# Performance work log

Hardware: AMD Instinct MI355X
Metric: run time of the kernel (lower is better)

The kernel has to match this reference:

```python
import jax, jax.numpy as jnp
import numpy as np

NUM_BINS = 16

def _compute_histogram(colors, num_bins=NUM_BINS):
    # colors: (N, 3) in [0, 1]
    quantized = (colors * (num_bins - 1)).astype(jnp.int32)
    quantized = jnp.clip(quantized, 0, num_bins - 1)
    # flatten 3D bin index: r*B^2 + g*B + b
    flat_idx = (quantized[:, 0] * num_bins + quantized[:, 1]) * num_bins + quantized[:, 2]
    hist = jax.ops.segment_sum(
        jnp.ones(colors.shape[0], dtype=colors.dtype),
        flat_idx,
        num_segments=num_bins ** 3,
    )
    hist = hist / (hist.sum() + 1e-8)
    return hist  # (num_bins^3,)

def setup_inputs() -> dict:
    key = jax.random.key(0)
    k1, k2 = jax.random.split(key)
    source_colors = jax.random.uniform(k1, (8388608, 3), dtype=jnp.float32)
    target_palette = jax.random.uniform(k2, (4096, 3), dtype=jnp.float32)
    return {"source_colors": source_colors, "target_palette": target_palette}

def reference(source_colors, target_palette):
    source_hist = _compute_histogram(source_colors)
    target_hist = _compute_histogram(target_palette)
    loss = jnp.abs(source_hist - target_hist).mean()
    return loss
```

## Files before the change

kernel.cpp:

```cpp
#include <hip/hip_runtime.h>

#define BINS 4096

__device__ __forceinline__ int qz(float c) {
    int q = (int)(c * 15.0f);
    q = q < 0 ? 0 : q;
    q = q > 15 ? 15 : q;
    return q;
}

__device__ __forceinline__ int bin3(float r, float g, float b) {
    return (qz(r) * 16 + qz(g)) * 16 + qz(b);
}

__global__ __launch_bounds__(256) void src_hist_kernel(const float* __restrict__ src,
                                                       unsigned int* __restrict__ g_hist,
                                                       int n_pts) {
    __shared__ unsigned int lhist[BINS];
    for (int i = threadIdx.x; i < BINS; i += blockDim.x) lhist[i] = 0;
    __syncthreads();

    const float4* __restrict__ src4 = (const float4*)src;
    const int n_quads = n_pts >> 2;
    const int tid = blockIdx.x * blockDim.x + threadIdx.x;
    const int stride = gridDim.x * blockDim.x;

    for (int q = tid; q < n_quads; q += stride) {
        float4 a = src4[3 * q + 0];
        float4 b = src4[3 * q + 1];
        float4 c = src4[3 * q + 2];
        atomicAdd(&lhist[bin3(a.x, a.y, a.z)], 1u);
        atomicAdd(&lhist[bin3(a.w, b.x, b.y)], 1u);
        atomicAdd(&lhist[bin3(b.z, b.w, c.x)], 1u);
        atomicAdd(&lhist[bin3(c.y, c.z, c.w)], 1u);
    }

    if (blockIdx.x == 0) {
        int tail = n_pts & 3;
        if ((int)threadIdx.x < tail) {
            int p = (n_quads << 2) + threadIdx.x;
            atomicAdd(&lhist[bin3(src[3 * p], src[3 * p + 1], src[3 * p + 2])], 1u);
        }
    }

    __syncthreads();
    for (int i = threadIdx.x; i < BINS; i += blockDim.x) {
        unsigned int v = lhist[i];
        if (v) atomicAdd(&g_hist[i], v);
    }
}

__global__ __launch_bounds__(512) void loss_kernel(const float* __restrict__ tgt,
                                                   const unsigned int* __restrict__ g_hist,
                                                   float* __restrict__ out,
                                                   int n_src, int n_tgt) {
    __shared__ unsigned int thist[BINS];
    for (int i = threadIdx.x; i < BINS; i += blockDim.x) thist[i] = 0;
    __syncthreads();

    const float4* __restrict__ t4 = (const float4*)tgt;
    const int n_quads = n_tgt >> 2;
    for (int q = threadIdx.x; q < n_quads; q += blockDim.x) {
        float4 a = t4[3 * q + 0];
        float4 b = t4[3 * q + 1];
        float4 c = t4[3 * q + 2];
        atomicAdd(&thist[bin3(a.x, a.y, a.z)], 1u);
        atomicAdd(&thist[bin3(a.w, b.x, b.y)], 1u);
        atomicAdd(&thist[bin3(b.z, b.w, c.x)], 1u);
        atomicAdd(&thist[bin3(c.y, c.z, c.w)], 1u);
    }
    {
        int tail = n_tgt & 3;
        if ((int)threadIdx.x < tail) {
            int p = (n_quads << 2) + threadIdx.x;
            atomicAdd(&thist[bin3(tgt[3 * p], tgt[3 * p + 1], tgt[3 * p + 2])], 1u);
        }
    }
    __syncthreads();

    const double ns = (double)n_src + 1e-8;
    const double nt = (double)n_tgt + 1e-8;
    double acc = 0.0;
    for (int i = threadIdx.x; i < BINS; i += blockDim.x) {
        double s = (double)g_hist[i] / ns;
        double t = (double)thist[i] / nt;
        acc += fabs(s - t);
    }

    for (int off = 32; off > 0; off >>= 1) acc += __shfl_down(acc, off);
    __shared__ double red[8];
    const int lane = threadIdx.x & 63;
    const int wave = threadIdx.x >> 6;
    if (lane == 0) red[wave] = acc;
    __syncthreads();
    if (threadIdx.x == 0) {
        double s = 0.0;
        const int nwaves = (int)(blockDim.x >> 6);
        for (int w = 0; w < nwaves; ++w) s += red[w];
        out[0] = (float)(s / (double)BINS);
    }
}

extern "C" void kernel_launch(void* const* d_in, const int* in_sizes, int n_in,
                              void* d_out, int out_size, void* d_ws, size_t ws_size,
                              hipStream_t stream) {
    const float* src = (const float*)d_in[0];
    const float* tgt = (const float*)d_in[1];
    const int n_src = in_sizes[0] / 3;
    const int n_tgt = in_sizes[1] / 3;

    unsigned int* g_hist = (unsigned int*)d_ws;

    hipMemsetAsync(g_hist, 0, BINS * sizeof(unsigned int), stream);
    src_hist_kernel<<<1024, 256, 0, stream>>>(src, g_hist, n_src);
    loss_kernel<<<1, 512, 0, stream>>>(tgt, g_hist, (float*)d_out, n_src, n_tgt);
}
```

Baseline: 164.5 us.

## Fuse source histogram and loss into one kernel with last-block finalize

Merges the two kernels into a single launch. The last block to finish, found through an atomic counter and threadfence, builds the target histogram and computes the loss. The grid changes from 1024x256 to 256x512, and each block's flush into the global histogram starts at a rotated offset to spread atomic contention across bins. This removes one kernel launch and the gap between kernels. In exchange it adds a serialized tail on a single block plus the fence and counter overhead.

Result: slower. 176.1 us (+7.0%).

```diff
diff --git a/kernel.cpp b/kernel.cpp
--- a/kernel.cpp
+++ b/kernel.cpp
@@ -1,6 +1,8 @@
 #include <hip/hip_runtime.h>
 
 #define BINS 4096
+#define GRID 256
+#define BLOCK 512
 
 __device__ __forceinline__ int qz(float c) {
     int q = (int)(c * 15.0f);
@@ -10,21 +12,21 @@
 }
 
 __device__ __forceinline__ int bin3(float r, float g, float b) {
-    return (qz(r) * 16 + qz(g)) * 16 + qz(b);
+    return (qz(r) << 8) | (qz(g) << 4) | qz(b);
 }
 
-__global__ __launch_bounds__(256) void src_hist_kernel(const float* __restrict__ src,
-                                                       unsigned int* __restrict__ g_hist,
-                                                       int n_pts) {
+__global__ __launch_bounds__(BLOCK) void fused_hist_loss_kernel(
+        const float* __restrict__ src, const float* __restrict__ tgt,
+        unsigned int* __restrict__ g_hist, unsigned int* __restrict__ counter,
+        float* __restrict__ out, int n_src, int n_tgt) {
     __shared__ unsigned int lhist[BINS];
-    for (int i = threadIdx.x; i < BINS; i += blockDim.x) lhist[i] = 0;
+    for (int i = threadIdx.x; i < BINS; i += BLOCK) lhist[i] = 0;
     __syncthreads();
 
     const float4* __restrict__ src4 = (const float4*)src;
-    const int n_quads = n_pts >> 2;
-    const int tid = blockIdx.x * blockDim.x + threadIdx.x;
-    const int stride = gridDim.x * blockDim.x;
-
+    const int n_quads = n_src >> 2;
+    const int tid = blockIdx.x * BLOCK + threadIdx.x;
+    const int stride = gridDim.x * BLOCK;
     for (int q = tid; q < n_quads; q += stride) {
         float4 a = src4[3 * q + 0];
         float4 b = src4[3 * q + 1];
@@ -34,46 +36,50 @@
         atomicAdd(&lhist[bin3(b.z, b.w, c.x)], 1u);
         atomicAdd(&lhist[bin3(c.y, c.z, c.w)], 1u);
     }
-
     if (blockIdx.x == 0) {
-        int tail = n_pts & 3;
+        int tail = n_src & 3;
         if ((int)threadIdx.x < tail) {
             int p = (n_quads << 2) + threadIdx.x;
             atomicAdd(&lhist[bin3(src[3 * p], src[3 * p + 1], src[3 * p + 2])], 1u);
         }
     }
+    __syncthreads();
 
-    __syncthreads();
-    for (int i = threadIdx.x; i < BINS; i += blockDim.x) {
+    const int rot = (blockIdx.x * 64) & (BINS - 1);
+    for (int k = threadIdx.x; k < BINS; k += BLOCK) {
+        int i = (k + rot) & (BINS - 1);
         unsigned int v = lhist[i];
         if (v) atomicAdd(&g_hist[i], v);
     }
-}
 
-__global__ __launch_bounds__(512) void loss_kernel(const float* __restrict__ tgt,
-                                                   const unsigned int* __restrict__ g_hist,
-                                                   float* __restrict__ out,
-                                                   int n_src, int n_tgt) {
-    __shared__ unsigned int thist[BINS];
-    for (int i = threadIdx.x; i < BINS; i += blockDim.x) thist[i] = 0;
+    __threadfence();
     __syncthreads();
+    __shared__ int is_last;
+    if (threadIdx.x == 0) {
+        unsigned int prev = atomicAdd(counter, 1u);
+        is_last = (prev == (unsigned int)(gridDim.x - 1)) ? 1 : 0;
+    }
+    __syncthreads();
+    if (!is_last) return;
 
+    for (int i = threadIdx.x; i < BINS; i += BLOCK) lhist[i] = 0;
+    __syncthreads();
     const float4* __restrict__ t4 = (const float4*)tgt;
-    const int n_quads = n_tgt >> 2;
-    for (int q = threadIdx.x; q < n_quads; q += blockDim.x) {
+    const int tq = n_tgt >> 2;
+    for (int q = threadIdx.x; q < tq; q += BLOCK) {
         float4 a = t4[3 * q + 0];
         float4 b = t4[3 * q + 1];
         float4 c = t4[3 * q + 2];
-        atomicAdd(&thist[bin3(a.x, a.y, a.z)], 1u);
-        atomicAdd(&thist[bin3(a.w, b.x, b.y)], 1u);
-        atomicAdd(&thist[bin3(b.z, b.w, c.x)], 1u);
-        atomicAdd(&thist[bin3(c.y, c.z, c.w)], 1u);
+        atomicAdd(&lhist[bin3(a.x, a.y, a.z)], 1u);
+        atomicAdd(&lhist[bin3(a.w, b.x, b.y)], 1u);
+        atomicAdd(&lhist[bin3(b.z, b.w, c.x)], 1u);
+        atomicAdd(&lhist[bin3(c.y, c.z, c.w)], 1u);
     }
     {
         int tail = n_tgt & 3;
         if ((int)threadIdx.x < tail) {
-            int p = (n_quads << 2) + threadIdx.x;
-            atomicAdd(&thist[bin3(tgt[3 * p], tgt[3 * p + 1], tgt[3 * p + 2])], 1u);
+            int p = (tq << 2) + threadIdx.x;
+            atomicAdd(&lhist[bin3(tgt[3 * p], tgt[3 * p + 1], tgt[3 * p + 2])], 1u);
         }
     }
     __syncthreads();
@@ -81,22 +87,21 @@
     const double ns = (double)n_src + 1e-8;
     const double nt = (double)n_tgt + 1e-8;
     double acc = 0.0;
-    for (int i = threadIdx.x; i < BINS; i += blockDim.x) {
-        double s = (double)g_hist[i] / ns;
-        double t = (double)thist[i] / nt;
+    for (int i = threadIdx.x; i < BINS; i += BLOCK) {
+        unsigned int sv = atomicAdd(&g_hist[i], 0u);
+        double s = (double)sv / ns;
+        double t = (double)lhist[i] / nt;
         acc += fabs(s - t);
     }
-
     for (int off = 32; off > 0; off >>= 1) acc += __shfl_down(acc, off);
-    __shared__ double red[8];
+    __shared__ double red[BLOCK / 64];
     const int lane = threadIdx.x & 63;
     const int wave = threadIdx.x >> 6;
     if (lane == 0) red[wave] = acc;
     __syncthreads();
     if (threadIdx.x == 0) {
         double s = 0.0;
-        const int nwaves = (int)(blockDim.x >> 6);
-        for (int w = 0; w < nwaves; ++w) s += red[w];
+        for (int w = 0; w < BLOCK / 64; ++w) s += red[w];
         out[0] = (float)(s / (double)BINS);
     }
 }
@@ -110,8 +115,9 @@
     const int n_tgt = in_sizes[1] / 3;
 
     unsigned int* g_hist = (unsigned int*)d_ws;
+    unsigned int* counter = g_hist + BINS;
 
-    hipMemsetAsync(g_hist, 0, BINS * sizeof(unsigned int), stream);
-    src_hist_kernel<<<1024, 256, 0, stream>>>(src, g_hist, n_src);
-    loss_kernel<<<1, 512, 0, stream>>>(tgt, g_hist, (float*)d_out, n_src, n_tgt);
+    hipMemsetAsync(d_ws, 0, (BINS + 16) * sizeof(unsigned int), stream);
+    fused_hist_loss_kernel<<<GRID, BLOCK, 0, stream>>>(
+        src, tgt, g_hist, counter, (float*)d_out, n_src, n_tgt);
 }
```

## Pack source histogram into 16-bit shared counters with per-block partials and reduction

Applied to the files above, without the earlier changes.

The source histogram now keeps two 16-bit counters per shared-memory word, which halves LDS use so more blocks fit per CU, and the grid doubles to 2048 blocks. Each block writes its packed partial histogram to global memory instead of doing global atomics, and a new reduce kernel sums the partials per bin, which also removes the memset. The loss kernel grows to 1024 threads. The risk is 16-bit counter overflow if one block sees more than 65535 points in a bin, plus the extra traffic and latency of a serial 2048-step reduction done by only 64 blocks.

Result: slower. 203.5 us (+23.7%).

```diff
diff --git a/kernel.cpp b/kernel.cpp
--- a/kernel.cpp
+++ b/kernel.cpp
@@ -1,6 +1,9 @@
 #include <hip/hip_runtime.h>
 
 #define BINS 4096
+#define WORDS 2048
+#define H_GRID 2048
+#define H_BLOCK 256
 
 __device__ __forceinline__ int qz(float c) {
     int q = (int)(c * 15.0f);
@@ -10,70 +13,84 @@
 }
 
 __device__ __forceinline__ int bin3(float r, float g, float b) {
-    return (qz(r) * 16 + qz(g)) * 16 + qz(b);
+    return (qz(r) << 8) | (qz(g) << 4) | qz(b);
 }
 
-__global__ __launch_bounds__(256) void src_hist_kernel(const float* __restrict__ src,
-                                                       unsigned int* __restrict__ g_hist,
-                                                       int n_pts) {
-    __shared__ unsigned int lhist[BINS];
-    for (int i = threadIdx.x; i < BINS; i += blockDim.x) lhist[i] = 0;
+__global__ __launch_bounds__(H_BLOCK) void hist_partial_kernel(
+        const float* __restrict__ src, unsigned int* __restrict__ partials,
+        int n_pts) {
+    __shared__ unsigned int lh[WORDS];
+    for (int i = threadIdx.x; i < WORDS; i += H_BLOCK) lh[i] = 0;
     __syncthreads();
 
     const float4* __restrict__ src4 = (const float4*)src;
     const int n_quads = n_pts >> 2;
-    const int tid = blockIdx.x * blockDim.x + threadIdx.x;
-    const int stride = gridDim.x * blockDim.x;
-
+    const int tid = blockIdx.x * H_BLOCK + threadIdx.x;
+    const int stride = gridDim.x * H_BLOCK;
     for (int q = tid; q < n_quads; q += stride) {
         float4 a = src4[3 * q + 0];
         float4 b = src4[3 * q + 1];
         float4 c = src4[3 * q + 2];
-        atomicAdd(&lhist[bin3(a.x, a.y, a.z)], 1u);
-        atomicAdd(&lhist[bin3(a.w, b.x, b.y)], 1u);
-        atomicAdd(&lhist[bin3(b.z, b.w, c.x)], 1u);
-        atomicAdd(&lhist[bin3(c.y, c.z, c.w)], 1u);
+        int b0 = bin3(a.x, a.y, a.z);
+        int b1 = bin3(a.w, b.x, b.y);
+        int b2 = bin3(b.z, b.w, c.x);
+        int b3 = bin3(c.y, c.z, c.w);
+        atomicAdd(&lh[b0 >> 1], 1u << ((b0 & 1) << 4));
+        atomicAdd(&lh[b1 >> 1], 1u << ((b1 & 1) << 4));
+        atomicAdd(&lh[b2 >> 1], 1u << ((b2 & 1) << 4));
+        atomicAdd(&lh[b3 >> 1], 1u << ((b3 & 1) << 4));
     }
-
     if (blockIdx.x == 0) {
         int tail = n_pts & 3;
         if ((int)threadIdx.x < tail) {
             int p = (n_quads << 2) + threadIdx.x;
-            atomicAdd(&lhist[bin3(src[3 * p], src[3 * p + 1], src[3 * p + 2])], 1u);
+            int bb = bin3(src[3 * p], src[3 * p + 1], src[3 * p + 2]);
+            atomicAdd(&lh[bb >> 1], 1u << ((bb & 1) << 4));
         }
     }
+    __syncthreads();
 
-    __syncthreads();
-    for (int i = threadIdx.x; i < BINS; i += blockDim.x) {
-        unsigned int v = lhist[i];
-        if (v) atomicAdd(&g_hist[i], v);
-    }
+    uint4* dst = (uint4*)(partials + (size_t)blockIdx.x * WORDS);
+    const uint4* lh4 = (const uint4*)lh;
+#pragma unroll
+    for (int p = 0; p < WORDS / (H_BLOCK * 4); ++p)
+        dst[threadIdx.x + p * H_BLOCK] = lh4[threadIdx.x + p * H_BLOCK];
 }
 
-__global__ __launch_bounds__(512) void loss_kernel(const float* __restrict__ tgt,
-                                                   const unsigned int* __restrict__ g_hist,
-                                                   float* __restrict__ out,
-                                                   int n_src, int n_tgt) {
-    __shared__ unsigned int thist[BINS];
-    for (int i = threadIdx.x; i < BINS; i += blockDim.x) thist[i] = 0;
+__global__ __launch_bounds__(64) void reduce_kernel(
+        const unsigned int* __restrict__ partials,
+        unsigned int* __restrict__ g_hist) {
+    const int bin = blockIdx.x * 64 + threadIdx.x;
+    const unsigned short* __restrict__ p16 = (const unsigned short*)partials;
+    unsigned int s = 0;
+    for (int b = 0; b < H_GRID; ++b)
+        s += (unsigned int)p16[(size_t)b * BINS + bin];
+    g_hist[bin] = s;
+}
+
+__global__ __launch_bounds__(1024) void loss_kernel(
+        const float* __restrict__ tgt, const unsigned int* __restrict__ g_hist,
+        float* __restrict__ out, int n_src, int n_tgt) {
+    __shared__ unsigned int th[BINS];
+    for (int i = threadIdx.x; i < BINS; i += 1024) th[i] = 0;
     __syncthreads();
 
     const float4* __restrict__ t4 = (const float4*)tgt;
-    const int n_quads = n_tgt >> 2;
-    for (int q = threadIdx.x; q < n_quads; q += blockDim.x) {
+    const int tq = n_tgt >> 2;
+    for (int q = threadIdx.x; q < tq; q += 1024) {
         float4 a = t4[3 * q + 0];
         float4 b = t4[3 * q + 1];
         float4 c = t4[3 * q + 2];
-        atomicAdd(&thist[bin3(a.x, a.y, a.z)], 1u);
-        atomicAdd(&thist[bin3(a.w, b.x, b.y)], 1u);
-        atomicAdd(&thist[bin3(b.z, b.w, c.x)], 1u);
-        atomicAdd(&thist[bin3(c.y, c.z, c.w)], 1u);
+        atomicAdd(&th[bin3(a.x, a.y, a.z)], 1u);
+        atomicAdd(&th[bin3(a.w, b.x, b.y)], 1u);
+        atomicAdd(&th[bin3(b.z, b.w, c.x)], 1u);
+        atomicAdd(&th[bin3(c.y, c.z, c.w)], 1u);
     }
     {
         int tail = n_tgt & 3;
         if ((int)threadIdx.x < tail) {
-            int p = (n_quads << 2) + threadIdx.x;
-            atomicAdd(&thist[bin3(tgt[3 * p], tgt[3 * p + 1], tgt[3 * p + 2])], 1u);
+            int p = (tq << 2) + threadIdx.x;
+            atomicAdd(&th[bin3(tgt[3 * p], tgt[3 * p + 1], tgt[3 * p + 2])], 1u);
         }
     }
     __syncthreads();
@@ -81,22 +98,16 @@
     const double ns = (double)n_src + 1e-8;
     const double nt = (double)n_tgt + 1e-8;
     double acc = 0.0;
-    for (int i = threadIdx.x; i < BINS; i += blockDim.x) {
-        double s = (double)g_hist[i] / ns;
-        double t = (double)thist[i] / nt;
-        acc += fabs(s - t);
-    }
+    for (int i = threadIdx.x; i < BINS; i += 1024)
+        acc += fabs((double)g_hist[i] / ns - (double)th[i] / nt);
 
     for (int off = 32; off > 0; off >>= 1) acc += __shfl_down(acc, off);
-    __shared__ double red[8];
-    const int lane = threadIdx.x & 63;
-    const int wave = threadIdx.x >> 6;
-    if (lane == 0) red[wave] = acc;
+    __shared__ double red[16];
+    if ((threadIdx.x & 63) == 0) red[threadIdx.x >> 6] = acc;
     __syncthreads();
     if (threadIdx.x == 0) {
         double s = 0.0;
-        const int nwaves = (int)(blockDim.x >> 6);
-        for (int w = 0; w < nwaves; ++w) s += red[w];
+        for (int w = 0; w < 16; ++w) s += red[w];
         out[0] = (float)(s / (double)BINS);
     }
 }
@@ -109,9 +120,10 @@
     const int n_src = in_sizes[0] / 3;
     const int n_tgt = in_sizes[1] / 3;
 
-    unsigned int* g_hist = (unsigned int*)d_ws;
+    unsigned int* partials = (unsigned int*)d_ws;
+    unsigned int* g_hist   = partials + (size_t)H_GRID * WORDS;
 
-    hipMemsetAsync(g_hist, 0, BINS * sizeof(unsigned int), stream);
-    src_hist_kernel<<<1024, 256, 0, stream>>>(src, g_hist, n_src);
-    loss_kernel<<<1, 512, 0, stream>>>(tgt, g_hist, (float*)d_out, n_src, n_tgt);
+    hist_partial_kernel<<<H_GRID, H_BLOCK, 0, stream>>>(src, partials, n_src);
+    reduce_kernel<<<BINS / 64, 64, 0, stream>>>(partials, g_hist);
+    loss_kernel<<<1, 1024, 0, stream>>>(tgt, g_hist, (float*)d_out, n_src, n_tgt);
 }
```
